# Kernel optimization log

Hardware: AMD Instinct MI355X
Metric: run time of the kernel (lower is better)

Reference implementation:

```python
import jax, jax.numpy as jnp
import numpy as np

N_SUBJECTS, C_IN, C_OUT = 128, 273, 273
B, T = 256, 360


def setup_inputs() -> dict:
    key = jax.random.key(0)
    k1, k2, k3 = jax.random.split(key, 3)
    x = jax.random.normal(k1, (B, C_IN, T), dtype=jnp.float32)
    subjects = jax.random.randint(k2, (B,), 0, N_SUBJECTS, dtype=jnp.int64)
    weights = jax.random.normal(k3, (N_SUBJECTS, C_IN, C_OUT), dtype=jnp.float32)
    return {"x": x, "subjects": subjects, "weights": weights}


def reference(x, subjects, weights):
    # Gather per-sample weight matrix: (B, C, D)
    w = weights[subjects]
    # bct,bcd -> bdt : per-sample channel remap applied at every timestep
    return jnp.einsum('bct,bcd->bdt', x, w)
```

## Files before the change

### kernel.cpp

```cpp
#include <hip/hip_runtime.h>
#include <hip/hip_bf16.h>

#define NBATCH 256
#define NC 273
#define ND 273
#define NT 360

#define THREADS 512
#define BM 288
#define BN 128
#define BNV 120
#define BK 32
#define LDK 40
#define KITERS 9

typedef __bf16 bf16_t;
typedef bf16_t bf16x4 __attribute__((ext_vector_type(4)));
typedef bf16_t bf16x8 __attribute__((ext_vector_type(8)));
typedef float  f32x4  __attribute__((ext_vector_type(4)));

#define LDS_FENCE_BARRIER()                                   \
    do {                                                      \
        asm volatile("s_waitcnt lgkmcnt(0)" ::: "memory");    \
        __builtin_amdgcn_s_barrier();                         \
    } while (0)

__global__ __launch_bounds__(THREADS, 2) void subject_gemm(
    const float* __restrict__ x,
    const int*   __restrict__ subjects,
    const float* __restrict__ w,
    float*       __restrict__ out)
{
    const int raw  = blockIdx.x;
    const int xcd  = raw & 7;
    const int slot = raw >> 3;
    const int b    = xcd * 32 + slot / 3;
    const int tt   = slot % 3;
    const int t0   = tt * BNV;
    const int s    = subjects[b];

    const float* __restrict__ xb = x + (size_t)b * NC * NT;
    const float* __restrict__ ws = w + (size_t)s * NC * ND;

    __shared__ __align__(16) bf16_t As[2][BM * LDK];
    __shared__ __align__(16) bf16_t Bs[2][BN * LDK];

    const int tid   = threadIdx.x;
    const int lane  = tid & 63;
    const int wid   = tid >> 6;
    const int wm    = wid >> 2;
    const int wn    = wid & 3;
    const int l16   = lane & 15;
    const int khalf = lane >> 4;

    int offA[5], gA[5];
#pragma unroll
    for (int j = 0; j < 5; ++j) {
        const int i  = tid + THREADS * j;
        const int ii = (i < 2304) ? i : 2303;
        const int d  = ii % BM;
        const int kq = ii / BM;
        offA[j] = d * LDK + kq * 4;
        gA[j]   = kq * 4 * ND + d;
    }
    int offB[2], gB[2];
#pragma unroll
    for (int j = 0; j < 2; ++j) {
        const int i  = tid + THREADS * j;
        const int t  = i & (BN - 1);
        const int kq = i >> 7;
        const int tc = (t < BNV) ? t : (BNV - 1);
        offB[j] = t * LDK + kq * 4;
        gB[j]   = kq * 4 * NT + t0 + tc;
    }
    const bool haveJ4 = (tid < 2304 - 4 * THREADS);

    float raA[5][4], raB[5][4], rbA[2][4], rbB[2][4];

    auto loadA = [&](float (&r)[5][4], int kk) {
        const int base = kk * ND;
#pragma unroll
        for (int j = 0; j < 4; ++j)
#pragma unroll
            for (int u = 0; u < 4; ++u)
                r[j][u] = ws[base + gA[j] + u * ND];
        if (haveJ4)
#pragma unroll
            for (int u = 0; u < 4; ++u)
                r[4][u] = ws[base + gA[4] + u * ND];
    };
    auto loadB = [&](float (&r)[2][4], int kk) {
        const int base = kk * NT;
#pragma unroll
        for (int j = 0; j < 2; ++j)
#pragma unroll
            for (int u = 0; u < 4; ++u)
                r[j][u] = xb[base + gB[j] + u * NT];
    };
    auto loadA_tail = [&](float (&r)[5][4]) {
#pragma unroll
        for (int j = 0; j < 5; ++j) {
            if (j == 4 && !haveJ4) break;
            const int i  = tid + THREADS * j;
            const int d  = i % BM;
            const int kq = i / BM;
#pragma unroll
            for (int u = 0; u < 4; ++u) {
                const int c = 256 + kq * 4 + u;
                const bool ok = (c < NC) && (d < ND);
                r[j][u] = ok ? ws[c * ND + d] : 0.f;
            }
        }
    };
    auto loadB_tail = [&](float (&r)[2][4]) {
#pragma unroll
        for (int j = 0; j < 2; ++j) {
            const int i  = tid + THREADS * j;
            const int t  = i & (BN - 1);
            const int kq = i >> 7;
            const int col = t0 + ((t < BNV) ? t : (BNV - 1));
#pragma unroll
            for (int u = 0; u < 4; ++u) {
                const int c  = 256 + kq * 4 + u;
                const int cc = (c < NC) ? c : (NC - 1);
                r[j][u] = xb[cc * NT + col];
            }
        }
    };
    auto stage = [&](const float (&rA)[5][4], const float (&rB)[2][4],
                     bf16_t* dA, bf16_t* dB) {
#pragma unroll
        for (int j = 0; j < 4; ++j) {
            bf16x4 v;
#pragma unroll
            for (int u = 0; u < 4; ++u) v[u] = (bf16_t)rA[j][u];
            *(bf16x4*)&dA[offA[j]] = v;
        }
        if (haveJ4) {
            bf16x4 v;
#pragma unroll
            for (int u = 0; u < 4; ++u) v[u] = (bf16_t)rA[4][u];
            *(bf16x4*)&dA[offA[4]] = v;
        }
#pragma unroll
        for (int j = 0; j < 2; ++j) {
            bf16x4 v;
#pragma unroll
            for (int u = 0; u < 4; ++u) v[u] = (bf16_t)rB[j][u];
            *(bf16x4*)&dB[offB[j]] = v;
        }
    };

    f32x4 acc[9][2];
#pragma unroll
    for (int m = 0; m < 9; ++m)
#pragma unroll
        for (int n = 0; n < 2; ++n)
            acc[m][n] = (f32x4){0.f, 0.f, 0.f, 0.f};

    auto compute = [&](const bf16_t* Ac, const bf16_t* Bc) {
        bf16x8 af[9], bfr[2];
#pragma unroll
        for (int n = 0; n < 2; ++n)
            bfr[n] = *(const bf16x8*)&Bc[(wn * 32 + n * 16 + l16) * LDK + khalf * 8];
#pragma unroll
        for (int m = 0; m < 9; ++m)
            af[m] = *(const bf16x8*)&Ac[(wm * 144 + m * 16 + l16) * LDK + khalf * 8];
#pragma unroll
        for (int m = 0; m < 9; ++m)
#pragma unroll
            for (int n = 0; n < 2; ++n)
                acc[m][n] = __builtin_amdgcn_mfma_f32_16x16x32_bf16(af[m], bfr[n], acc[m][n], 0, 0, 0);
    };

    loadA(raA, 0);      loadB(rbA, 0);
    loadA(raB, BK);     loadB(rbB, BK);
    stage(raA, rbA, &As[0][0], &Bs[0][0]);
    LDS_FENCE_BARRIER();

#pragma unroll
    for (int p = 0; p < 4; ++p) {
        const int it0 = 2 * p;
        {
            bf16x8 af[9], bfr[2];
#pragma unroll
            for (int n = 0; n < 2; ++n)
                bfr[n] = *(const bf16x8*)&Bs[0][(wn * 32 + n * 16 + l16) * LDK + khalf * 8];
#pragma unroll
            for (int m = 0; m < 9; ++m)
                af[m] = *(const bf16x8*)&As[0][(wm * 144 + m * 16 + l16) * LDK + khalf * 8];

            if (it0 + 2 <= KITERS - 2) {
                loadA(raA, (it0 + 2) * BK);
                loadB(rbA, (it0 + 2) * BK);
            } else if (it0 + 2 == KITERS - 1) {
                loadA_tail(raA);
                loadB_tail(rbA);
            }
            stage(raB, rbB, &As[1][0], &Bs[1][0]);
            LDS_FENCE_BARRIER();

#pragma unroll
            for (int m = 0; m < 9; ++m)
#pragma unroll
                for (int n = 0; n < 2; ++n)
                    acc[m][n] = __builtin_amdgcn_mfma_f32_16x16x32_bf16(af[m], bfr[n], acc[m][n], 0, 0, 0);
        }
        const int it1 = 2 * p + 1;
        {
            bf16x8 af[9], bfr[2];
#pragma unroll
            for (int n = 0; n < 2; ++n)
                bfr[n] = *(const bf16x8*)&Bs[1][(wn * 32 + n * 16 + l16) * LDK + khalf * 8];
#pragma unroll
            for (int m = 0; m < 9; ++m)
                af[m] = *(const bf16x8*)&As[1][(wm * 144 + m * 16 + l16) * LDK + khalf * 8];

            if (it1 + 2 <= KITERS - 2) {
                loadA(raB, (it1 + 2) * BK);
                loadB(rbB, (it1 + 2) * BK);
            }
            stage(raA, rbA, &As[0][0], &Bs[0][0]);
            LDS_FENCE_BARRIER();

#pragma unroll
            for (int m = 0; m < 9; ++m)
#pragma unroll
                for (int n = 0; n < 2; ++n)
                    acc[m][n] = __builtin_amdgcn_mfma_f32_16x16x32_bf16(af[m], bfr[n], acc[m][n], 0, 0, 0);
        }
    }
    compute(&As[0][0], &Bs[0][0]);

    float* __restrict__ ob = out + (size_t)b * ND * NT;
#pragma unroll
    for (int m = 0; m < 9; ++m) {
#pragma unroll
        for (int n = 0; n < 2; ++n) {
            const int tc = wn * 32 + n * 16 + l16;
            const int gt = t0 + tc;
#pragma unroll
            for (int rg = 0; rg < 4; ++rg) {
                const int d = wm * 144 + m * 16 + khalf * 4 + rg;
                if (d < ND && tc < BNV)
                    ob[(size_t)d * NT + gt] = acc[m][n][rg];
            }
        }
    }
}

extern "C" void kernel_launch(void* const* d_in, const int* in_sizes, int n_in,
                              void* d_out, int out_size, void* d_ws, size_t ws_size,
                              hipStream_t stream) {
    const float* x        = (const float*)d_in[0];
    const int*   subjects = (const int*)d_in[1];
    const float* w        = (const float*)d_in[2];
    float*       out      = (float*)d_out;

    const int nblocks = NBATCH * 3;
    subject_gemm<<<nblocks, THREADS, 0, stream>>>(x, subjects, w, out);
}
```

Before: 60.12 us.

## Pre-transpose and convert subject weights to padded bf16 in workspace

Adds a pre-pass kernel that transposes each subject's weight matrix into a zero-padded 288x288 bf16 layout in the workspace. The GEMM kernel then loads A tiles as contiguous bf16x4 vectors, with no per-element strided fp32 loads or conversion, and needs no special tail load. This halves weight traffic in the main kernel and makes those loads coalesced along K. The cost is an extra launch that converts all 128 subjects' weights on every call, including ones that are never used, and a fallback path is kept for when the workspace is too small.

```diff
diff --git a/kernel.cpp b/kernel.cpp
--- a/kernel.cpp
+++ b/kernel.cpp
@@ -5,6 +5,7 @@
 #define NC 273
 #define ND 273
 #define NT 360
+#define NSUB 128
 
 #define THREADS 512
 #define BM 288
@@ -14,6 +15,10 @@
 #define LDK 40
 #define KITERS 9
 
+#define WT_LD 288
+#define WT_SUBJ (288 * 288)
+#define WT_BYTES ((size_t)NSUB * WT_SUBJ * 2)
+
 typedef __bf16 bf16_t;
 typedef bf16_t bf16x4 __attribute__((ext_vector_type(4)));
 typedef bf16_t bf16x8 __attribute__((ext_vector_type(8)));
@@ -25,11 +30,42 @@
         __builtin_amdgcn_s_barrier();                         \
     } while (0)
 
+__global__ __launch_bounds__(256) void conv_w(const float* __restrict__ w,
+                                              bf16_t* __restrict__ wT) {
+    const int bid  = blockIdx.x;
+    const int s    = bid / 25;
+    const int tile = bid % 25;
+    const int c0   = (tile / 5) * 64;
+    const int d0   = (tile % 5) * 64;
+    const int tx   = threadIdx.x & 63;
+    const int ty   = threadIdx.x >> 6;
+
+    __shared__ float t[64][65];
+    const float* __restrict__ wsrc = w + (size_t)s * NC * ND;
+#pragma unroll
+    for (int j = 0; j < 16; ++j) {
+        const int row = ty + j * 4;
+        const int c = c0 + row, d = d0 + tx;
+        t[row][tx] = (c < NC && d < ND) ? wsrc[c * ND + d] : 0.f;
+    }
+    __syncthreads();
+    bf16_t* __restrict__ wdst = wT + (size_t)s * WT_SUBJ;
+#pragma unroll
+    for (int j = 0; j < 16; ++j) {
+        const int row = ty + j * 4;
+        const int d = d0 + row, c = c0 + tx;
+        if (d < ND && c < WT_LD)
+            wdst[d * WT_LD + c] = (bf16_t)t[tx][row];
+    }
+}
+
+template<bool BF16W>
 __global__ __launch_bounds__(THREADS, 2) void subject_gemm(
-    const float* __restrict__ x,
-    const int*   __restrict__ subjects,
-    const float* __restrict__ w,
-    float*       __restrict__ out)
+    const float*  __restrict__ x,
+    const int*    __restrict__ subjects,
+    const float*  __restrict__ w,
+    const bf16_t* __restrict__ wT,
+    float*        __restrict__ out)
 {
     const int raw  = blockIdx.x;
     const int xcd  = raw & 7;
@@ -39,8 +75,9 @@
     const int t0   = tt * BNV;
     const int s    = subjects[b];
 
-    const float* __restrict__ xb = x + (size_t)b * NC * NT;
-    const float* __restrict__ ws = w + (size_t)s * NC * ND;
+    const float*  __restrict__ xb  = x  + (size_t)b * NC * NT;
+    const float*  __restrict__ wsf = w  + (size_t)s * NC * ND;
+    const bf16_t* __restrict__ wsb = wT + (size_t)s * WT_SUBJ;
 
     __shared__ __align__(16) bf16_t As[2][BM * LDK];
     __shared__ __align__(16) bf16_t Bs[2][BN * LDK];
@@ -58,10 +95,11 @@
     for (int j = 0; j < 5; ++j) {
         const int i  = tid + THREADS * j;
         const int ii = (i < 2304) ? i : 2303;
-        const int d  = ii % BM;
-        const int kq = ii / BM;
+        const int kq = ii & 7;
+        const int d  = ii >> 3;
         offA[j] = d * LDK + kq * 4;
-        gA[j]   = kq * 4 * ND + d;
+        gA[j]   = BF16W ? (d * WT_LD + kq * 4)
+                        : (kq * 4 * ND + d);
     }
     int offB[2], gB[2];
 #pragma unroll
@@ -75,19 +113,32 @@
     }
     const bool haveJ4 = (tid < 2304 - 4 * THREADS);
 
-    float raA[5][4], raB[5][4], rbA[2][4], rbB[2][4];
-
-    auto loadA = [&](float (&r)[5][4], int kk) {
-        const int base = kk * ND;
-#pragma unroll
-        for (int j = 0; j < 4; ++j)
-#pragma unroll
-            for (int u = 0; u < 4; ++u)
-                r[j][u] = ws[base + gA[j] + u * ND];
-        if (haveJ4)
-#pragma unroll
-            for (int u = 0; u < 4; ++u)
-                r[4][u] = ws[base + gA[4] + u * ND];
+    bf16x4 aEv[5], aOd[5];
+    float  bEv[2][4], bOd[2][4];
+
+    auto loadA = [&](bf16x4 (&r)[5], int kk) {
+        if constexpr (BF16W) {
+#pragma unroll
+            for (int j = 0; j < 4; ++j)
+                r[j] = *(const bf16x4*)&wsb[gA[j] + kk];
+            if (haveJ4)
+                r[4] = *(const bf16x4*)&wsb[gA[4] + kk];
+        } else {
+#pragma unroll
+            for (int j = 0; j < 5; ++j) {
+                if (j == 4 && !haveJ4) break;
+                const int i  = tid + THREADS * j;
+                const int ii = (i < 2304) ? i : 2303;
+                const int kq = ii & 7;
+                const int d  = ii >> 3;
+#pragma unroll
+                for (int u = 0; u < 4; ++u) {
+                    const int c = kk + kq * 4 + u;
+                    const float f = (c < NC && d < ND) ? wsf[c * ND + d] : 0.f;
+                    r[j][u] = (bf16_t)f;
+                }
+            }
+        }
     };
     auto loadB = [&](float (&r)[2][4], int kk) {
         const int base = kk * NT;
@@ -96,21 +147,6 @@
 #pragma unroll
             for (int u = 0; u < 4; ++u)
                 r[j][u] = xb[base + gB[j] + u * NT];
-    };
-    auto loadA_tail = [&](float (&r)[5][4]) {
-#pragma unroll
-        for (int j = 0; j < 5; ++j) {
-            if (j == 4 && !haveJ4) break;
-            const int i  = tid + THREADS * j;
-            const int d  = i % BM;
-            const int kq = i / BM;
-#pragma unroll
-            for (int u = 0; u < 4; ++u) {
-                const int c = 256 + kq * 4 + u;
-                const bool ok = (c < NC) && (d < ND);
-                r[j][u] = ok ? ws[c * ND + d] : 0.f;
-            }
-        }
     };
     auto loadB_tail = [&](float (&r)[2][4]) {
 #pragma unroll
@@ -127,21 +163,13 @@
             }
         }
     };
-    auto stage = [&](const float (&rA)[5][4], const float (&rB)[2][4],
+    auto stage = [&](const bf16x4 (&rA)[5], const float (&rB)[2][4],
                      bf16_t* dA, bf16_t* dB) {
 #pragma unroll
-        for (int j = 0; j < 4; ++j) {
-            bf16x4 v;
-#pragma unroll
-            for (int u = 0; u < 4; ++u) v[u] = (bf16_t)rA[j][u];
-            *(bf16x4*)&dA[offA[j]] = v;
-        }
-        if (haveJ4) {
-            bf16x4 v;
-#pragma unroll
-            for (int u = 0; u < 4; ++u) v[u] = (bf16_t)rA[4][u];
-            *(bf16x4*)&dA[offA[4]] = v;
-        }
+        for (int j = 0; j < 4; ++j)
+            *(bf16x4*)&dA[offA[j]] = rA[j];
+        if (haveJ4)
+            *(bf16x4*)&dA[offA[4]] = rA[4];
 #pragma unroll
         for (int j = 0; j < 2; ++j) {
             bf16x4 v;
@@ -158,79 +186,75 @@
         for (int n = 0; n < 2; ++n)
             acc[m][n] = (f32x4){0.f, 0.f, 0.f, 0.f};
 
-    auto compute = [&](const bf16_t* Ac, const bf16_t* Bc) {
+    loadA(aEv, 0);       loadB(bEv, 0);
+    loadA(aOd, BK);      loadB(bOd, BK);
+    stage(aEv, bEv, &As[0][0], &Bs[0][0]);
+    LDS_FENCE_BARRIER();
+
+#pragma unroll
+    for (int p = 0; p < 4; ++p) {
+        {
+            const int it0 = 2 * p;
+            bf16x8 af[9], bfr[2];
+#pragma unroll
+            for (int n = 0; n < 2; ++n)
+                bfr[n] = *(const bf16x8*)&Bs[0][(wn * 32 + n * 16 + l16) * LDK + khalf * 8];
+#pragma unroll
+            for (int m = 0; m < 9; ++m)
+                af[m] = *(const bf16x8*)&As[0][(wm * 144 + m * 16 + l16) * LDK + khalf * 8];
+
+            if (it0 + 2 <= KITERS - 1) {
+                loadA(aEv, (it0 + 2) * BK);
+                if (it0 + 2 <= KITERS - 2) loadB(bEv, (it0 + 2) * BK);
+                else                       loadB_tail(bEv);
+            }
+            stage(aOd, bOd, &As[1][0], &Bs[1][0]);
+            LDS_FENCE_BARRIER();
+
+#pragma unroll
+            for (int m = 0; m < 9; ++m)
+#pragma unroll
+                for (int n = 0; n < 2; ++n)
+                    acc[m][n] = __builtin_amdgcn_mfma_f32_16x16x32_bf16(af[m], bfr[n], acc[m][n], 0, 0, 0);
+        }
+        {
+            const int it1 = 2 * p + 1;
+            bf16x8 af[9], bfr[2];
+#pragma unroll
+            for (int n = 0; n < 2; ++n)
+                bfr[n] = *(const bf16x8*)&Bs[1][(wn * 32 + n * 16 + l16) * LDK + khalf * 8];
+#pragma unroll
+            for (int m = 0; m < 9; ++m)
+                af[m] = *(const bf16x8*)&As[1][(wm * 144 + m * 16 + l16) * LDK + khalf * 8];
+
+            if (it1 + 2 <= KITERS - 2) {
+                loadA(aOd, (it1 + 2) * BK);
+                loadB(bOd, (it1 + 2) * BK);
+            }
+            stage(aEv, bEv, &As[0][0], &Bs[0][0]);
+            LDS_FENCE_BARRIER();
+
+#pragma unroll
+            for (int m = 0; m < 9; ++m)
+#pragma unroll
+                for (int n = 0; n < 2; ++n)
+                    acc[m][n] = __builtin_amdgcn_mfma_f32_16x16x32_bf16(af[m], bfr[n], acc[m][n], 0, 0, 0);
+        }
+    }
+    {
         bf16x8 af[9], bfr[2];
 #pragma unroll
         for (int n = 0; n < 2; ++n)
-            bfr[n] = *(const bf16x8*)&Bc[(wn * 32 + n * 16 + l16) * LDK + khalf * 8];
+            bfr[n] = *(const bf16x8*)&Bs[0][(wn * 32 + n * 16 + l16) * LDK + khalf * 8];
 #pragma unroll
         for (int m = 0; m < 9; ++m)
-            af[m] = *(const bf16x8*)&Ac[(wm * 144 + m * 16 + l16) * LDK + khalf * 8];
+            af[m] = *(const bf16x8*)&As[0][(wm * 144 + m * 16 + l16) * LDK + khalf * 8];
 #pragma unroll
         for (int m = 0; m < 9; ++m)
 #pragma unroll
             for (int n = 0; n < 2; ++n)
                 acc[m][n] = __builtin_amdgcn_mfma_f32_16x16x32_bf16(af[m], bfr[n], acc[m][n], 0, 0, 0);
-    };
-
-    loadA(raA, 0);      loadB(rbA, 0);
-    loadA(raB, BK);     loadB(rbB, BK);
-    stage(raA, rbA, &As[0][0], &Bs[0][0]);
-    LDS_FENCE_BARRIER();
-
-#pragma unroll
-    for (int p = 0; p < 4; ++p) {
-        const int it0 = 2 * p;
-        {
-            bf16x8 af[9], bfr[2];
-#pragma unroll
-            for (int n = 0; n < 2; ++n)
-                bfr[n] = *(const bf16x8*)&Bs[0][(wn * 32 + n * 16 + l16) * LDK + khalf * 8];
-#pragma unroll
-            for (int m = 0; m < 9; ++m)
-                af[m] = *(const bf16x8*)&As[0][(wm * 144 + m * 16 + l16) * LDK + khalf * 8];
-
-            if (it0 + 2 <= KITERS - 2) {
-                loadA(raA, (it0 + 2) * BK);
-                loadB(rbA, (it0 + 2) * BK);
-            } else if (it0 + 2 == KITERS - 1) {
-                loadA_tail(raA);
-                loadB_tail(rbA);
-            }
-            stage(raB, rbB, &As[1][0], &Bs[1][0]);
-            LDS_FENCE_BARRIER();
-
-#pragma unroll
-            for (int m = 0; m < 9; ++m)
-#pragma unroll
-                for (int n = 0; n < 2; ++n)
-                    acc[m][n] = __builtin_amdgcn_mfma_f32_16x16x32_bf16(af[m], bfr[n], acc[m][n], 0, 0, 0);
-        }
-        const int it1 = 2 * p + 1;
-        {
-            bf16x8 af[9], bfr[2];
-#pragma unroll
-            for (int n = 0; n < 2; ++n)
-                bfr[n] = *(const bf16x8*)&Bs[1][(wn * 32 + n * 16 + l16) * LDK + khalf * 8];
-#pragma unroll
-            for (int m = 0; m < 9; ++m)
-                af[m] = *(const bf16x8*)&As[1][(wm * 144 + m * 16 + l16) * LDK + khalf * 8];
-
-            if (it1 + 2 <= KITERS - 2) {
-                loadA(raB, (it1 + 2) * BK);
-                loadB(rbB, (it1 + 2) * BK);
-            }
-            stage(raA, rbA, &As[0][0], &Bs[0][0]);
-            LDS_FENCE_BARRIER();
-
-#pragma unroll
-            for (int m = 0; m < 9; ++m)
-#pragma unroll
-                for (int n = 0; n < 2; ++n)
-                    acc[m][n] = __builtin_amdgcn_mfma_f32_16x16x32_bf16(af[m], bfr[n], acc[m][n], 0, 0, 0);
-        }
-    }
-    compute(&As[0][0], &Bs[0][0]);
+    }
 
     float* __restrict__ ob = out + (size_t)b * ND * NT;
 #pragma unroll
@@ -256,7 +280,14 @@
     const int*   subjects = (const int*)d_in[1];
     const float* w        = (const float*)d_in[2];
     float*       out      = (float*)d_out;
+    bf16_t*      wT       = (bf16_t*)d_ws;
 
     const int nblocks = NBATCH * 3;
-    subject_gemm<<<nblocks, THREADS, 0, stream>>>(x, subjects, w, out);
+
+    if (ws_size >= WT_BYTES) {
+        conv_w<<<NSUB * 25, 256, 0, stream>>>(w, wT);
+        subject_gemm<true><<<nblocks, THREADS, 0, stream>>>(x, subjects, w, wT, out);
+    } else {
+        subject_gemm<false><<<nblocks, THREADS, 0, stream>>>(x, subjects, w, wT, out);
+    }
 }
```

Measured after the change: 69.73 us. 16.0% more time.
